# Performance work log

Hardware: AMD Instinct MI355X
Metric: run time of the kernel (lower is better)

Reference implementation:

```python
import jax, jax.numpy as jnp
import numpy as np

B, S, H, NH = 2, 2048, 2048, 16
HD = H // NH  # head_dim = 128


def setup_inputs() -> dict:
    key = jax.random.key(0)
    ks = jax.random.split(key, 6)
    scale = 1.0 / np.sqrt(H)
    hidden_state = jax.random.normal(ks[0], (B, S, H), dtype=jnp.float32)
    # upper-triangular (strictly above diagonal) = 1 -> masked positions
    causal_mask = jnp.triu(jnp.ones((S, S), dtype=jnp.float32), k=1)[None, None]
    Wq = jax.random.normal(ks[1], (H, H), dtype=jnp.float32) * scale
    Wk = jax.random.normal(ks[2], (H, H), dtype=jnp.float32) * scale
    Wv = jax.random.normal(ks[3], (H, H), dtype=jnp.float32) * scale
    Wo = jax.random.normal(ks[4], (H, H), dtype=jnp.float32) * scale
    zeros = jnp.zeros((H,), dtype=jnp.float32)
    return {"hidden_state": hidden_state, "causal_mask": causal_mask,
            "Wq": Wq, "bq": zeros, "Wk": Wk, "bk": zeros,
            "Wv": Wv, "bv": zeros, "Wo": Wo, "bo": zeros}


def reference(hidden_state, causal_mask, Wq, bq, Wk, bk, Wv, bv, Wo, bo):
    b, s, h = hidden_state.shape
    q = (hidden_state @ Wq.T + bq).reshape(b, s, NH, HD).transpose(0, 2, 1, 3)  # [B,NH,S,HD]
    k = (hidden_state @ Wk.T + bk).reshape(b, s, NH, HD).transpose(0, 2, 1, 3)
    v = (hidden_state @ Wv.T + bv).reshape(b, s, NH, HD).transpose(0, 2, 1, 3)
    scores = jnp.einsum('bhqd,bhkd->bhqk', q, k) / jnp.sqrt(jnp.float32(HD))
    scores = scores + causal_mask * (-1e9)
    probs = jax.nn.softmax(scores, axis=-1)
    out = jnp.einsum('bhqk,bhkd->bhqd', probs, v)
    out = out.transpose(0, 2, 1, 3).reshape(b, s, h)
    return out @ Wo.T + bo
```

## Files before the change

### kernel.cpp

```cpp
#include <hip/hip_runtime.h>
#include <hip/hip_bf16.h>
#include <stdint.h>

#define B_   2
#define S_   2048
#define H_   2048
#define NH_  16
#define HD_  128
#define MTOT (B_*S_)

typedef __attribute__((ext_vector_type(8))) short bf16x8;
typedef __attribute__((ext_vector_type(4))) short bf16x4;
typedef __attribute__((ext_vector_type(4))) float f32x4;

__device__ __forceinline__ void gload_lds16(const void* g, void* l) {
    __builtin_amdgcn_global_load_lds(
        (const __attribute__((address_space(1))) void*)g,
        (__attribute__((address_space(3))) void*)l, 16, 0, 0);
}

__device__ __forceinline__ unsigned short f2bfu(float x) {
    __hip_bfloat16 h = __float2bfloat16(x);
    return *reinterpret_cast<unsigned short*>(&h);
}
__device__ __forceinline__ int packbf(float a, float b) {
    return (int)f2bfu(a) | ((int)f2bfu(b) << 16);
}

#define BAR()  asm volatile("s_barrier" ::: "memory")
#define WLG0() asm volatile("s_waitcnt lgkmcnt(0)" ::: "memory")
#define WVM(n) asm volatile("s_waitcnt vmcnt(" #n ")" ::: "memory")

__global__ void castk(const float* __restrict__ in, __hip_bfloat16* __restrict__ out, int n4) {
    int i = blockIdx.x * 256 + threadIdx.x;
    if (i < n4) {
        float4 v = *(const float4*)(in + (size_t)i * 4);
        out[(size_t)i*4 + 0] = __float2bfloat16(v.x);
        out[(size_t)i*4 + 1] = __float2bfloat16(v.y);
        out[(size_t)i*4 + 2] = __float2bfloat16(v.z);
        out[(size_t)i*4 + 3] = __float2bfloat16(v.w);
    }
}

__global__ void castw4(const float* __restrict__ w0, const float* __restrict__ w1,
                       const float* __restrict__ w2, const float* __restrict__ w3,
                       __hip_bfloat16* o0, __hip_bfloat16* o1,
                       __hip_bfloat16* o2, __hip_bfloat16* o3, int n4) {
    const float* in; __hip_bfloat16* out;
    switch (blockIdx.y) {
        case 0:  in = w0; out = o0; break;
        case 1:  in = w1; out = o1; break;
        case 2:  in = w2; out = o2; break;
        default: in = w3; out = o3; break;
    }
    int i = blockIdx.x * 256 + threadIdx.x;
    if (i < n4) {
        float4 v = *(const float4*)(in + (size_t)i * 4);
        out[(size_t)i*4 + 0] = __float2bfloat16(v.x);
        out[(size_t)i*4 + 1] = __float2bfloat16(v.y);
        out[(size_t)i*4 + 2] = __float2bfloat16(v.z);
        out[(size_t)i*4 + 3] = __float2bfloat16(v.w);
    }
}

template<int EPI>
__device__ __forceinline__ void gemm256_body(const __hip_bfloat16* __restrict__ Xp,
                                             const __hip_bfloat16* __restrict__ Wp,
                                             const float* __restrict__ bias,
                                             void* __restrict__ Cout,
                                             int bm, int bn, char* smem)
{
    const int tid  = threadIdx.x;
    const int wave = tid >> 6, lane = tid & 63;
    const int quad = lane >> 4, l16 = lane & 15;
    const int wr = wave >> 2, wc = wave & 3;

    const int ro = l16 * 64;
    const int co = (((l16 & 8) ? ((quad * 8) ^ 16) : (quad * 8)) << 1);

    int r0, c0, r1, c1;
    {
        int D = tid * 16;
        int rg = D >> 11, cg = (D >> 10) & 1;
        int rr = (D >> 6) & 15, c = (D & 63) >> 1;
        int cs = (rr & 8) ? (c ^ 16) : c;
        r0 = rg * 16 + rr;  c0 = cg * 32 + cs;
        D = 8192 + tid * 16;
        rg = D >> 11; cg = (D >> 10) & 1;
        rr = (D >> 6) & 15; c = (D & 63) >> 1;
        cs = (rr & 8) ? (c ^ 16) : c;
        r1 = rg * 16 + rr;  c1 = cg * 32 + cs;
    }

    char* const A0h = smem + wr * 16384;
    char* const A1h = smem + 32768 + wr * 16384;
    char* const B0h = smem + 65536 + (wc >> 1) * 16384;
    char* const B1h = smem + 98304 + (wc >> 1) * 16384;
    const int bsub = (wc & 1) * 4;

    auto STG = [&](char* ldsb, const __hip_bfloat16* g) {
        gload_lds16(g + (size_t)r0 * H_ + c0, ldsb + wave * 1024);
        gload_lds16(g + (size_t)r1 * H_ + c1, ldsb + 8192 + wave * 1024);
    };
    auto SRC = [&](const __hip_bfloat16* P, int t, int hf) {
        return P + (size_t)(hf * 128) * H_ + (size_t)t * 64;
    };

    f32x4 acc[8][4] = {};

    STG(smem,                 SRC(Xp, 0, 0));
    STG(smem + 16384,         SRC(Xp, 0, 1));
    STG(smem + 65536,         SRC(Wp, 0, 0));
    STG(smem + 65536 + 16384, SRC(Wp, 0, 1));
    STG(smem + 98304,         SRC(Wp, 1, 0));
    STG(smem + 98304 + 16384, SRC(Wp, 1, 1));
    WVM(4);
    BAR();

    const int NIT = H_ / 128;
    bf16x8 bfr[4][2];
    for (int j = 0; j < NIT; ++j) {
        const bool more = (j < NIT - 1);
        const int t1 = 2 * j + 1;
#pragma unroll
        for (int ph = 0; ph < 8; ++ph) {
            const int p = ph & 3;
            char* aA = (ph < 4) ? A0h : A1h;
            char* aB = (ph < 4) ? B0h : B1h;

            if (p == 0) {
#pragma unroll
                for (int jj = 0; jj < 4; ++jj)
#pragma unroll
                    for (int kk = 0; kk < 2; ++kk)
                        bfr[jj][kk] = *(const bf16x8*)(aB + ((bsub + jj) * 2 + kk) * 1024 + ro + co);
            }
            bf16x8 af[2][2];
#pragma unroll
            for (int i2 = 0; i2 < 2; ++i2)
#pragma unroll
                for (int kk = 0; kk < 2; ++kk)
                    af[i2][kk] = *(const bf16x8*)(aA + ((2 * p + i2) * 2 + kk) * 1024 + ro + co);

            if (ph == 0) { STG(smem + 32768, SRC(Xp, t1, 0));
                           STG(smem + 49152, SRC(Xp, t1, 1)); }
            else if (ph == 1 && more) STG(smem + 65536,          SRC(Wp, t1 + 1, 0));
            else if (ph == 2 && more) STG(smem + 65536 + 16384,  SRC(Wp, t1 + 1, 1));
            else if (ph == 4 && more) STG(smem,                  SRC(Xp, t1 + 1, 0));
            else if (ph == 5 && more) STG(smem + 16384,          SRC(Xp, t1 + 1, 1));
            else if (ph == 6 && more) STG(smem + 98304,          SRC(Wp, t1 + 2, 0));
            else if (ph == 7 && more) STG(smem + 98304 + 16384,  SRC(Wp, t1 + 2, 1));

            if (ph == 3) { if (more) { WVM(4); } else { WVM(0); } }
            if (ph == 7 && more) { WVM(4); }

            BAR();
            WLG0();
            __builtin_amdgcn_sched_barrier(0);
            __builtin_amdgcn_s_setprio(1);
#pragma unroll
            for (int kk = 0; kk < 2; ++kk)
#pragma unroll
                for (int i2 = 0; i2 < 2; ++i2)
#pragma unroll
                    for (int jj = 0; jj < 4; ++jj)
                        acc[2 * p + i2][jj] = __builtin_amdgcn_mfma_f32_16x16x32_bf16(
                            af[i2][kk], bfr[jj][kk], acc[2 * p + i2][jj], 0, 0, 0);
            __builtin_amdgcn_s_setprio(0);
            BAR();
        }
    }

    if (EPI == 2) {
        __hip_bfloat16* VTo = (__hip_bfloat16*)Cout;
#pragma unroll
        for (int i = 0; i < 8; ++i) {
            int tok = bm * 256 + wr * 128 + i * 16 + quad * 4;
            int b = tok >> 11, s = tok & (S_ - 1);
#pragma unroll
            for (int jj = 0; jj < 4; ++jj) {
                int col = bn * 256 + wc * 64 + jj * 16 + l16;
                int h = col >> 7, d = col & 127;
                float bv = bias[col];
                bf16x4 v;
#pragma unroll
                for (int r = 0; r < 4; ++r)
                    v[r] = (short)f2bfu(acc[i][jj][r] + bv);
                *(bf16x4*)(VTo + ((size_t)(b * 16 + h) * 128 + d) * S_ + s) = v;
            }
        }
    } else {
#pragma unroll
        for (int i = 0; i < 8; ++i) {
            int row = bm * 256 + wr * 128 + i * 16 + quad * 4;
#pragma unroll
            for (int jj = 0; jj < 4; ++jj) {
                int col = bn * 256 + wc * 64 + jj * 16 + l16;
                float bv = bias[col];
#pragma unroll
                for (int r = 0; r < 4; ++r) {
                    float v = acc[i][jj][r] + bv;
                    if (EPI == 1)
                        ((__hip_bfloat16*)Cout)[(size_t)(row + r) * H_ + col] = __float2bfloat16(v);
                    else
                        ((float*)Cout)[(size_t)(row + r) * H_ + col] = v;
                }
            }
        }
    }
}

__global__ __launch_bounds__(512, 2)
void gemm_qkv8(const __hip_bfloat16* __restrict__ X,
               const __hip_bfloat16* __restrict__ Wq, const __hip_bfloat16* __restrict__ Wk,
               const __hip_bfloat16* __restrict__ Wv,
               const float* __restrict__ bq, const float* __restrict__ bk,
               const float* __restrict__ bv,
               __hip_bfloat16* __restrict__ Qo, __hip_bfloat16* __restrict__ Ko,
               __hip_bfloat16* __restrict__ VTo)
{
    __shared__ __align__(16) char smem[131072];

    const int bid = blockIdx.x;
    const int swz = (bid & 7) * 48 + (bid >> 3);
    const int sel = swz >> 7;
    const int rem = swz & 127;
    const int bm  = rem & 15;
    const int bn  = rem >> 4;

    const __hip_bfloat16* W = (sel == 0) ? Wq : (sel == 1) ? Wk : Wv;
    const float* bias       = (sel == 0) ? bq : (sel == 1) ? bk : bv;

    const __hip_bfloat16* Xp = X + (size_t)(bm * 256) * H_;
    const __hip_bfloat16* Wp = W + (size_t)(bn * 256) * H_;

    if (sel == 2)
        gemm256_body<2>(Xp, Wp, bias, VTo, bm, bn, smem);
    else
        gemm256_body<1>(Xp, Wp, bias, (sel == 0) ? Qo : Ko, bm, bn, smem);
}

__global__ __launch_bounds__(512, 2)
void gemm_out8(const __hip_bfloat16* __restrict__ A, const __hip_bfloat16* __restrict__ W,
               const float* __restrict__ bias, float* __restrict__ C)
{
    __shared__ __align__(16) char smem[131072];
    const int bid = blockIdx.x;
    const int xcd = bid & 7, i = bid >> 3;
    const int bm  = (xcd & 3) * 4 + (i & 3);
    const int bn  = (xcd >> 2) * 4 + (i >> 2);
    gemm256_body<0>(A + (size_t)(bm * 256) * H_, W + (size_t)(bn * 256) * H_,
                    bias, C, bm, bn, smem);
}

__global__ __launch_bounds__(256)
void attn_kernel(const __hip_bfloat16* __restrict__ Q,
                 const __hip_bfloat16* __restrict__ K,
                 const __hip_bfloat16* __restrict__ VT,
                 __hip_bfloat16* __restrict__ O)
{
    __shared__ __align__(16) char Ks[16384];
    __shared__ __align__(16) char Vt[16384];

    const int tid  = threadIdx.x;
    const int wave = tid >> 6, lane = tid & 63;
    const int quad = lane >> 4, l16 = lane & 15;

    const int lid = blockIdx.x;
    const int xcd = lid & 7;
    const int q   = lid >> 3;
    const int bh  = ((q >> 5) << 3) | xcd;
    const int qb  = 31 - (q & 31);
    const int b   = bh >> 4, h = bh & 15;

    const size_t headoff = (size_t)b * S_ * H_ + (size_t)h * HD_;
    const __hip_bfloat16* Qp  = Q + headoff;
    const __hip_bfloat16* Kp  = K + headoff;
    const __hip_bfloat16* Vtp = VT + (size_t)(b * 16 + h) * 128 * S_;

    const float scale = 0.08838834764831843f;
    const int A0 = (((quad & 1) * 2) * 16 + l16) * 4;
    const int A1 = A0 + 64;
    const bool hiq = (quad >= 2);

    const int qrow_local = wave * 16;
    const int qrow = qb * 64 + qrow_local;

    bf16x8 qf[4];
#pragma unroll
    for (int kd = 0; kd < 4; ++kd)
        qf[kd] = *(const bf16x8*)(Qp + (size_t)(qrow + l16) * H_ + kd * 32 + quad * 8);

    f32x4 oacc[8] = {};
    float mi = -1e30f, li = 0.0f;

#pragma unroll
    for (int t = 0; t < 4; ++t) {
        int c = wave * 256 + t * 64 + lane;
        int krow = c >> 4, kpos = c & 15;
        gload_lds16(Kp + (size_t)krow * H_ + (kpos ^ (krow & 7)) * 8,
                    &Ks[(wave * 256 + t * 64) * 16]);
        int vrow = c >> 3, vpos = c & 7;
        gload_lds16(Vtp + (size_t)vrow * S_ + (vpos ^ (vrow & 7)) * 8,
                    &Vt[(wave * 256 + t * 64) * 16]);
    }
    __syncthreads();

    for (int kb = 0; kb <= qb; ++kb) {
        const bool more = (kb < qb);

        f32x4 sacc[4] = {};
#pragma unroll
        for (int cb = 0; cb < 4; ++cb) {
#pragma unroll
            for (int kd = 0; kd < 4; ++kd) {
                int row = cb * 16 + l16;
                int pos = (4 * kd + quad) ^ (l16 & 7);
                bf16x8 kf = *(const bf16x8*)&Ks[row * 256 + pos * 16];
                sacc[cb] = __builtin_amdgcn_mfma_f32_16x16x32_bf16(kf, qf[kd], sacc[cb], 0, 0, 0);
            }
        }

        __syncthreads();

        if (more) {
            const __hip_bfloat16* Kn = Kp + (size_t)(kb + 1) * 64 * H_;
#pragma unroll
            for (int t = 0; t < 4; ++t) {
                int c = wave * 256 + t * 64 + lane;
                int krow = c >> 4, kpos = c & 15;
                gload_lds16(Kn + (size_t)krow * H_ + (kpos ^ (krow & 7)) * 8,
                            &Ks[(wave * 256 + t * 64) * 16]);
            }
        }

        const bool diag = (kb == qb);
        float p[4][4];
        float tm = -1e30f;
#pragma unroll
        for (int cb = 0; cb < 4; ++cb)
#pragma unroll
            for (int r = 0; r < 4; ++r) {
                float s = sacc[cb][r] * scale;
                if (diag) {
                    int keyl = cb * 16 + quad * 4 + r;
                    if (keyl > qrow_local + l16) s = -1e30f;
                }
                p[cb][r] = s;
                tm = fmaxf(tm, s);
            }
        tm = fmaxf(tm, __shfl_xor(tm, 16));
        tm = fmaxf(tm, __shfl_xor(tm, 32));
        float mnew = fmaxf(mi, tm);
        float sum = 0.0f;
#pragma unroll
        for (int cb = 0; cb < 4; ++cb)
#pragma unroll
            for (int r = 0; r < 4; ++r) {
                float e = __expf(p[cb][r] - mnew);
                p[cb][r] = e;
                sum += e;
            }
        sum += __shfl_xor(sum, 16);
        sum += __shfl_xor(sum, 32);
        float alpha = __expf(mi - mnew);
        li = li * alpha + sum;
        mi = mnew;

        float ar[4];
#pragma unroll
        for (int r = 0; r < 4; ++r)
            ar[r] = __shfl(alpha, quad * 4 + r);
#pragma unroll
        for (int db = 0; db < 8; ++db)
#pragma unroll
            for (int r = 0; r < 4; ++r)
                oacc[db][r] *= ar[r];

        int Pp[4][2];
#pragma unroll
        for (int cb = 0; cb < 4; ++cb) {
            Pp[cb][0] = packbf(p[cb][0], p[cb][1]);
            Pp[cb][1] = packbf(p[cb][2], p[cb][3]);
        }
        bf16x8 pf[2];
#pragma unroll
        for (int ks = 0; ks < 2; ++ks) {
            int c0 = 2 * ks, c1 = 2 * ks + 1;
            int d0 = __builtin_amdgcn_ds_bpermute(A0, Pp[c0][0]);
            int e0 = __builtin_amdgcn_ds_bpermute(A0, Pp[c1][0]);
            int d1 = __builtin_amdgcn_ds_bpermute(A0, Pp[c0][1]);
            int e1 = __builtin_amdgcn_ds_bpermute(A0, Pp[c1][1]);
            int d2 = __builtin_amdgcn_ds_bpermute(A1, Pp[c0][0]);
            int e2 = __builtin_amdgcn_ds_bpermute(A1, Pp[c1][0]);
            int d3 = __builtin_amdgcn_ds_bpermute(A1, Pp[c0][1]);
            int e3 = __builtin_amdgcn_ds_bpermute(A1, Pp[c1][1]);
            union { int i[4]; bf16x8 v; } u;
            u.i[0] = hiq ? e0 : d0;
            u.i[1] = hiq ? e1 : d1;
            u.i[2] = hiq ? e2 : d2;
            u.i[3] = hiq ? e3 : d3;
            pf[ks] = u.v;
        }

#pragma unroll
        for (int ks = 0; ks < 2; ++ks) {
#pragma unroll
            for (int db = 0; db < 8; ++db) {
                int vrow = db * 16 + l16;
                int vpos = (ks * 4 + quad) ^ (l16 & 7);
                bf16x8 vf = *(const bf16x8*)&Vt[vrow * 128 + vpos * 16];
                oacc[db] = __builtin_amdgcn_mfma_f32_16x16x32_bf16(pf[ks], vf, oacc[db], 0, 0, 0);
            }
        }

        __syncthreads();

        if (more) {
            const int vcol = (kb + 1) * 64;
#pragma unroll
            for (int t = 0; t < 4; ++t) {
                int c = wave * 256 + t * 64 + lane;
                int vrow = c >> 3, vpos = c & 7;
                gload_lds16(Vtp + (size_t)vrow * S_ + vcol + (vpos ^ (vrow & 7)) * 8,
                            &Vt[(wave * 256 + t * 64) * 16]);
            }
        }
    }

    float lr[4];
#pragma unroll
    for (int r = 0; r < 4; ++r)
        lr[r] = __shfl(li, quad * 4 + r);
#pragma unroll
    for (int db = 0; db < 8; ++db)
#pragma unroll
        for (int r = 0; r < 4; ++r) {
            float v = oacc[db][r] / lr[r];
            size_t row = (size_t)b * S_ + qrow + quad * 4 + r;
            O[row * H_ + h * HD_ + db * 16 + l16] = __float2bfloat16(v);
        }
}

extern "C" void kernel_launch(void* const* d_in, const int* in_sizes, int n_in,
                              void* d_out, int out_size, void* d_ws, size_t ws_size,
                              hipStream_t stream)
{
    const float* hs = (const float*)d_in[0];
    const float* Wq = (const float*)d_in[2];
    const float* bq = (const float*)d_in[3];
    const float* Wk = (const float*)d_in[4];
    const float* bk = (const float*)d_in[5];
    const float* Wv = (const float*)d_in[6];
    const float* bv = (const float*)d_in[7];
    const float* Wo = (const float*)d_in[8];
    const float* bo = (const float*)d_in[9];

    const size_t szX = (size_t)MTOT * H_;
    const size_t szW = (size_t)H_ * H_;

    __hip_bfloat16* Xbf = (__hip_bfloat16*)d_ws;
    __hip_bfloat16* Wqb = Xbf + szX;
    __hip_bfloat16* Wkb = Wqb + szW;
    __hip_bfloat16* Wvb = Wkb + szW;
    __hip_bfloat16* Wob = Wvb + szW;
    __hip_bfloat16* Qb  = Wob + szW;
    __hip_bfloat16* Kb  = Qb + szX;
    __hip_bfloat16* VTb = Kb + szX;

    castk<<<(int)((szX/4 + 255)/256), 256, 0, stream>>>(hs, Xbf, (int)(szX/4));
    dim3 wgrid((unsigned)((szW/4 + 255)/256), 4);
    castw4<<<wgrid, 256, 0, stream>>>(Wq, Wk, Wv, Wo, Wqb, Wkb, Wvb, Wob, (int)(szW/4));

    gemm_qkv8<<<dim3(384), 512, 0, stream>>>(Xbf, Wqb, Wkb, Wvb, bq, bk, bv, Qb, Kb, VTb);

    attn_kernel<<<dim3(1024), 256, 0, stream>>>(Qb, Kb, VTb, Xbf);

    gemm_out8<<<dim3(128), 512, 0, stream>>>(Xbf, Wob, bo, (float*)d_out);
}
```

Before: 419.6 us.

## Merge cast kernels, split-K the output GEMM, and skip softmax rescale

Measured after the change: 412.3 us. About the same (-1.7%).

```diff
diff --git a/kernel.cpp b/kernel.cpp
--- a/kernel.cpp
+++ b/kernel.cpp
@@ -31,36 +31,30 @@
 #define WLG0() asm volatile("s_waitcnt lgkmcnt(0)" ::: "memory")
 #define WVM(n) asm volatile("s_waitcnt vmcnt(" #n ")" ::: "memory")
 
-__global__ void castk(const float* __restrict__ in, __hip_bfloat16* __restrict__ out, int n4) {
-    int i = blockIdx.x * 256 + threadIdx.x;
-    if (i < n4) {
-        float4 v = *(const float4*)(in + (size_t)i * 4);
-        out[(size_t)i*4 + 0] = __float2bfloat16(v.x);
-        out[(size_t)i*4 + 1] = __float2bfloat16(v.y);
-        out[(size_t)i*4 + 2] = __float2bfloat16(v.z);
-        out[(size_t)i*4 + 3] = __float2bfloat16(v.w);
-    }
-}
-
-__global__ void castw4(const float* __restrict__ w0, const float* __restrict__ w1,
-                       const float* __restrict__ w2, const float* __restrict__ w3,
-                       __hip_bfloat16* o0, __hip_bfloat16* o1,
-                       __hip_bfloat16* o2, __hip_bfloat16* o3, int n4) {
-    const float* in; __hip_bfloat16* out;
+__global__ void castall(const float* __restrict__ hs,
+                        const float* __restrict__ w0, const float* __restrict__ w1,
+                        const float* __restrict__ w2, const float* __restrict__ w3,
+                        __hip_bfloat16* __restrict__ xb,
+                        __hip_bfloat16* __restrict__ o0, __hip_bfloat16* __restrict__ o1,
+                        __hip_bfloat16* __restrict__ o2, __hip_bfloat16* __restrict__ o3)
+{
+    const size_t Q = 1048576;
+    const float* in; __hip_bfloat16* out; size_t base;
     switch (blockIdx.y) {
-        case 0:  in = w0; out = o0; break;
-        case 1:  in = w1; out = o1; break;
-        case 2:  in = w2; out = o2; break;
-        default: in = w3; out = o3; break;
-    }
-    int i = blockIdx.x * 256 + threadIdx.x;
-    if (i < n4) {
-        float4 v = *(const float4*)(in + (size_t)i * 4);
-        out[(size_t)i*4 + 0] = __float2bfloat16(v.x);
-        out[(size_t)i*4 + 1] = __float2bfloat16(v.y);
-        out[(size_t)i*4 + 2] = __float2bfloat16(v.z);
-        out[(size_t)i*4 + 3] = __float2bfloat16(v.w);
-    }
+        case 0:  in = hs; out = xb; base = 0; break;
+        case 1:  in = hs; out = xb; base = Q; break;
+        case 2:  in = w0; out = o0; base = 0; break;
+        case 3:  in = w1; out = o1; break;
+        case 4:  in = w2; out = o2; base = 0; break;
+        default: in = w3; out = o3; base = 0; break;
+    }
+    if (blockIdx.y == 3) base = 0;
+    size_t i = base + (size_t)blockIdx.x * 256 + threadIdx.x;
+    float4 v = *(const float4*)(in + i * 4);
+    uint2 o;
+    o.x = (unsigned)packbf(v.x, v.y);
+    o.y = (unsigned)packbf(v.z, v.w);
+    *(uint2*)((char*)out + i * 8) = o;
 }
 
 template<int EPI>
@@ -68,7 +62,7 @@
                                              const __hip_bfloat16* __restrict__ Wp,
                                              const float* __restrict__ bias,
                                              void* __restrict__ Cout,
-                                             int bm, int bn, char* smem)
+                                             int bm, int bn, char* smem, int NIT)
 {
     const int tid  = threadIdx.x;
     const int wave = tid >> 6, lane = tid & 63;
@@ -117,7 +111,6 @@
     WVM(4);
     BAR();
 
-    const int NIT = H_ / 128;
     bf16x8 bfr[4][2];
     for (int j = 0; j < NIT; ++j) {
         const bool more = (j < NIT - 1);
@@ -196,7 +189,7 @@
 #pragma unroll
             for (int jj = 0; jj < 4; ++jj) {
                 int col = bn * 256 + wc * 64 + jj * 16 + l16;
-                float bv = bias[col];
+                float bv = (EPI == 3) ? 0.0f : bias[col];
 #pragma unroll
                 for (int r = 0; r < 4; ++r) {
                     float v = acc[i][jj][r] + bv;
@@ -235,22 +228,39 @@
     const __hip_bfloat16* Wp = W + (size_t)(bn * 256) * H_;
 
     if (sel == 2)
-        gemm256_body<2>(Xp, Wp, bias, VTo, bm, bn, smem);
+        gemm256_body<2>(Xp, Wp, bias, VTo, bm, bn, smem, H_ / 128);
     else
-        gemm256_body<1>(Xp, Wp, bias, (sel == 0) ? Qo : Ko, bm, bn, smem);
+        gemm256_body<1>(Xp, Wp, bias, (sel == 0) ? Qo : Ko, bm, bn, smem, H_ / 128);
 }
 
 __global__ __launch_bounds__(512, 2)
-void gemm_out8(const __hip_bfloat16* __restrict__ A, const __hip_bfloat16* __restrict__ W,
-               const float* __restrict__ bias, float* __restrict__ C)
+void gemm_out8s(const __hip_bfloat16* __restrict__ A, const __hip_bfloat16* __restrict__ W,
+                const float* __restrict__ bias, float* __restrict__ C0, float* __restrict__ C1)
 {
     __shared__ __align__(16) char smem[131072];
     const int bid = blockIdx.x;
-    const int xcd = bid & 7, i = bid >> 3;
-    const int bm  = (xcd & 3) * 4 + (i & 3);
-    const int bn  = (xcd >> 2) * 4 + (i >> 2);
-    gemm256_body<0>(A + (size_t)(bm * 256) * H_, W + (size_t)(bn * 256) * H_,
-                    bias, C, bm, bn, smem);
+    const int swz = (bid & 7) * 32 + (bid >> 3);
+    const int kh  = swz >> 7;
+    const int rem = swz & 127;
+    const int bm  = rem & 15;
+    const int bn  = rem >> 4;
+
+    const __hip_bfloat16* Ap = A + (size_t)(bm * 256) * H_ + kh * 1024;
+    const __hip_bfloat16* Wp = W + (size_t)(bn * 256) * H_ + kh * 1024;
+
+    if (kh == 0)
+        gemm256_body<3>(Ap, Wp, bias, C0, bm, bn, smem, 8);
+    else
+        gemm256_body<0>(Ap, Wp, bias, C1, bm, bn, smem, 8);
+}
+
+__global__ void addred(const float* __restrict__ part, float* __restrict__ out)
+{
+    size_t i = ((size_t)blockIdx.x * 256 + threadIdx.x) * 4;
+    float4 a = *(const float4*)(out + i);
+    float4 b = *(const float4*)(part + i);
+    a.x += b.x; a.y += b.y; a.z += b.z; a.w += b.w;
+    *(float4*)(out + i) = a;
 }
 
 __global__ __launch_bounds__(256)
@@ -351,7 +361,10 @@
             }
         tm = fmaxf(tm, __shfl_xor(tm, 16));
         tm = fmaxf(tm, __shfl_xor(tm, 32));
-        float mnew = fmaxf(mi, tm);
+
+        const bool noresc = __all(tm - mi <= 8.0f);
+        float mnew = noresc ? mi : fmaxf(mi, tm);
+
         float sum = 0.0f;
 #pragma unroll
         for (int cb = 0; cb < 4; ++cb)
@@ -363,19 +376,23 @@
             }
         sum += __shfl_xor(sum, 16);
         sum += __shfl_xor(sum, 32);
-        float alpha = __expf(mi - mnew);
-        li = li * alpha + sum;
+
+        if (noresc) {
+            li = li + sum;
+        } else {
+            float alpha = __expf(mi - mnew);
+            li = li * alpha + sum;
+            float ar[4];
+#pragma unroll
+            for (int r = 0; r < 4; ++r)
+                ar[r] = __shfl(alpha, quad * 4 + r);
+#pragma unroll
+            for (int db = 0; db < 8; ++db)
+#pragma unroll
+                for (int r = 0; r < 4; ++r)
+                    oacc[db][r] *= ar[r];
+        }
         mi = mnew;
-
-        float ar[4];
-#pragma unroll
-        for (int r = 0; r < 4; ++r)
-            ar[r] = __shfl(alpha, quad * 4 + r);
-#pragma unroll
-        for (int db = 0; db < 8; ++db)
-#pragma unroll
-            for (int r = 0; r < 4; ++r)
-                oacc[db][r] *= ar[r];
 
         int Pp[4][2];
 #pragma unroll
@@ -468,13 +485,15 @@
     __hip_bfloat16* Kb  = Qb + szX;
     __hip_bfloat16* VTb = Kb + szX;
 
-    castk<<<(int)((szX/4 + 255)/256), 256, 0, stream>>>(hs, Xbf, (int)(szX/4));
-    dim3 wgrid((unsigned)((szW/4 + 255)/256), 4);
-    castw4<<<wgrid, 256, 0, stream>>>(Wq, Wk, Wv, Wo, Wqb, Wkb, Wvb, Wob, (int)(szW/4));
+    float* C0 = (float*)Qb;
+
+    castall<<<dim3(4096, 6), 256, 0, stream>>>(hs, Wq, Wk, Wv, Wo, Xbf, Wqb, Wkb, Wvb, Wob);
 
     gemm_qkv8<<<dim3(384), 512, 0, stream>>>(Xbf, Wqb, Wkb, Wvb, bq, bk, bv, Qb, Kb, VTb);
 
     attn_kernel<<<dim3(1024), 256, 0, stream>>>(Qb, Kb, VTb, Xbf);
 
-    gemm_out8<<<dim3(128), 512, 0, stream>>>(Xbf, Wob, bo, (float*)d_out);
-}
+    gemm_out8s<<<dim3(256), 512, 0, stream>>>(Xbf, Wob, bo, C0, (float*)d_out);
+
+    addred<<<dim3(8192), 256, 0, stream>>>(C0, (float*)d_out);
+}
```
